# Optimization experiments

Hardware: AMD Instinct MI355X
Metric: run time of the kernel (lower is better)

Reference implementation:

```python
import jax, jax.numpy as jnp
import numpy as np

B, Hm, Wm, Dm = 1, 32, 32, 32
N = Hm * Wm * Dm
C = 128
HEADS, DH = 8, 16
G = 32
L = 2
OUT = 1


def _ln(x, g, b):
    mu = jnp.mean(x, -1, keepdims=True)
    var = jnp.mean((x - mu) ** 2, -1, keepdims=True)
    return (x - mu) * jax.lax.rsqrt(var + 1e-5) * g + b


def setup_inputs() -> dict:
    key = jax.random.key(0)
    ks = iter(jax.random.split(key, 64))
    def nrm(shape, s=0.02):
        return jax.random.normal(next(ks), shape, jnp.float32) * s
    return {
        "x": jax.random.normal(next(ks), (B, N, 3), jnp.float32),
        "fx": jax.random.normal(next(ks), (B, N, 1), jnp.float32),
        "pre_w1": nrm((4, 2 * C)), "pre_b1": jnp.zeros((2 * C,), jnp.float32),
        "pre_w2": nrm((2 * C, C)), "pre_b2": jnp.zeros((C,), jnp.float32),
        "placeholder": jax.random.uniform(next(ks), (C,), jnp.float32) / C,
        "ln1_g": jnp.ones((L, C), jnp.float32), "ln1_b": jnp.zeros((L, C), jnp.float32),
        "convx_w": nrm((L, C, C, 3, 3, 3)), "convx_b": jnp.zeros((L, C), jnp.float32),
        "convfx_w": nrm((L, C, C, 3, 3, 3)), "convfx_b": jnp.zeros((L, C), jnp.float32),
        "slice_w": nrm((L, DH, G), 0.1), "slice_b": jnp.zeros((L, G), jnp.float32),
        "temperature": jnp.full((L, 1, HEADS, 1, 1), 0.5, jnp.float32),
        "wq": nrm((L, DH, DH), 0.1), "wk": nrm((L, DH, DH), 0.1), "wv": nrm((L, DH, DH), 0.1),
        "wo": nrm((L, HEADS * DH, C)), "bo": jnp.zeros((L, C), jnp.float32),
        "ln2_g": jnp.ones((L, C), jnp.float32), "ln2_b": jnp.zeros((L, C), jnp.float32),
        "mlp_w1": nrm((L, C, C)), "mlp_b1": jnp.zeros((L, C), jnp.float32),
        "mlp_w2": nrm((L, C, C)), "mlp_b2": jnp.zeros((L, C), jnp.float32),
        "ln3_g": jnp.ones((C,), jnp.float32), "ln3_b": jnp.zeros((C,), jnp.float32),
        "out_w": nrm((C, OUT)), "out_b": jnp.zeros((OUT,), jnp.float32),
    }


def _conv3d(x, w, b):
    # x: [B,C,H,W,D], w: [O,I,3,3,3], SAME padding (kernel//2) as torch Conv3d
    y = jax.lax.conv_general_dilated(x, w, (1, 1, 1), "SAME",
                                     dimension_numbers=("NCDHW", "OIDHW", "NCDHW"))
    return y + b[None, :, None, None, None]


def _physics_attn(z, cw_x, cb_x, cw_fx, cb_fx, sw, sb, temp, wq, wk, wv, wo, bo):
    # z: [B, N, C] -> structured mesh conv projections -> slice attention
    xg = z.reshape(B, Hm, Wm, Dm, C).transpose(0, 4, 1, 2, 3)  # [B,C,H,W,D]

    def split_heads(t):  # [B,I,H,W,D] -> [B,heads,N,dh]
        return t.transpose(0, 2, 3, 4, 1).reshape(B, N, HEADS, DH).transpose(0, 2, 1, 3)

    x_mid = split_heads(_conv3d(xg, cw_x, cb_x))
    fx_mid = split_heads(_conv3d(xg, cw_fx, cb_fx))
    # slice assignment weights: [B,heads,N,G], temperature-scaled softmax
    slice_logits = (x_mid @ sw + sb) / temp
    swt = jax.nn.softmax(slice_logits, axis=-1)
    norm = jnp.sum(swt, axis=2)  # [B,heads,G]
    tok = jnp.einsum("bhnc,bhng->bhgc", fx_mid, swt) / (norm + 1e-5)[..., None]
    q, k, v = tok @ wq, tok @ wk, tok @ wv  # [B,heads,G,dh]
    attn = jax.nn.softmax((q @ k.transpose(0, 1, 3, 2)) * (DH ** -0.5), axis=-1)
    ot = attn @ v  # [B,heads,G,dh]
    out = jnp.einsum("bhgc,bhng->bhnc", ot, swt)  # de-slice back to tokens
    out = out.transpose(0, 2, 1, 3).reshape(B, N, HEADS * DH)
    return out @ wo + bo


def reference(x, fx, pre_w1, pre_b1, pre_w2, pre_b2, placeholder,
              ln1_g, ln1_b, convx_w, convx_b, convfx_w, convfx_b,
              slice_w, slice_b, temperature, wq, wk, wv, wo, bo,
              ln2_g, ln2_b, mlp_w1, mlp_b1, mlp_w2, mlp_b2,
              ln3_g, ln3_b, out_w, out_b):
    h = jnp.concatenate([x, fx], axis=-1)  # [B,N,space+fun]
    z = jax.nn.gelu(h @ pre_w1 + pre_b1, approximate=False) @ pre_w2 + pre_b2 + placeholder
    for l in range(L):
        zn = _ln(z, ln1_g[l], ln1_b[l])
        z = _physics_attn(zn, convx_w[l], convx_b[l], convfx_w[l], convfx_b[l],
                          slice_w[l], slice_b[l], temperature[l],
                          wq[l], wk[l], wv[l], wo[l], bo[l]) + z
        zn = _ln(z, ln2_g[l], ln2_b[l])
        z = jax.nn.gelu(zn @ mlp_w1[l] + mlp_b1[l], approximate=False) @ mlp_w2[l] + mlp_b2[l] + z
    return _ln(z, ln3_g, ln3_b) @ out_w + out_b
```

## Files before the change

kernel.cpp:

```cpp
#include <hip/hip_runtime.h>
#include <hip/hip_bf16.h>

#define DEV __device__ __forceinline__

constexpr int N   = 32768;
constexpr int TOTAL_IN = 2038481;

constexpr int OFF_X        = 0;
constexpr int OFF_FX       = 98304;
constexpr int OFF_PRE_W1   = 131072;
constexpr int OFF_PRE_B1   = 132096;
constexpr int OFF_PRE_W2   = 132352;
constexpr int OFF_PRE_B2   = 165120;
constexpr int OFF_PLACE    = 165248;
constexpr int OFF_LN1_G    = 165376;
constexpr int OFF_LN1_B    = 165632;
constexpr int OFF_CONVX_W  = 165888;
constexpr int OFF_CONVX_B  = 1050624;
constexpr int OFF_CONVFX_W = 1050880;
constexpr int OFF_CONVFX_B = 1935616;
constexpr int OFF_SLICE_W  = 1935872;
constexpr int OFF_SLICE_B  = 1936896;
constexpr int OFF_TEMP     = 1936960;
constexpr int OFF_WQ       = 1936976;
constexpr int OFF_WK       = 1937488;
constexpr int OFF_WV       = 1938000;
constexpr int OFF_WO       = 1938512;
constexpr int OFF_BO       = 1971280;
constexpr int OFF_LN2_G    = 1971536;
constexpr int OFF_LN2_B    = 1971792;
constexpr int OFF_MLP_W1   = 1972048;
constexpr int OFF_MLP_B1   = 2004816;
constexpr int OFF_MLP_W2   = 2005072;
constexpr int OFF_MLP_B2   = 2037840;
constexpr int OFF_LN3_G    = 2038096;
constexpr int OFF_LN3_B    = 2038224;
constexpr int OFF_OUT_W    = 2038352;
constexpr int OFF_OUT_B    = 2038480;

__device__ __constant__ int d_PRE[32] = {
  0, 98304, 131072, 132096, 132352, 165120, 165248, 165376, 165632,
  165888, 1050624, 1050880, 1935616, 1935872, 1936896, 1936960, 1936976,
  1937488, 1938000, 1938512, 1971280, 1971536, 1971792, 1972048, 2004816,
  2005072, 2037840, 2038096, 2038224, 2038352, 2038480, 2038481
};

constexpr size_t F_IN   = 16;
constexpr size_t F_WT   = 2038512;
constexpr size_t F_Z    = F_WT   + 1769472;
constexpr size_t F_ZN   = F_Z    + 4194304;
constexpr size_t F_CONV = F_ZN   + 4194304;
constexpr size_t F_SWT  = F_CONV + 8388608;
constexpr size_t F_TOKP = F_SWT  + 8388608;
constexpr size_t F_TOK2 = F_TOKP + 1114112;
constexpr size_t F_WP   = F_TOK2 + 34816;
constexpr size_t F_END  = F_WP   + 65536;

struct InPtrs { const void* p[31]; };

typedef short short8v  __attribute__((ext_vector_type(8)));
typedef float float4v  __attribute__((ext_vector_type(4)));
#define MFMA16(A,B,C) __builtin_amdgcn_mfma_f32_16x16x32_bf16(A,B,C,0,0,0)

DEV float geluf(float x) { return 0.5f * x * (1.0f + erff(x * 0.70710678118654752f)); }
DEV short f2bs(float x) { union { __hip_bfloat16 h; short s; } c; c.h = __float2bfloat16(x); return c.s; }

__global__ void k_setup(InPtrs ptrs, float* __restrict__ ws,
                        short* __restrict__ wtf, short* __restrict__ wp) {
  const bool isbf = (*(const unsigned*)ptrs.p[15] == 0x3F003F00u);
  int b = blockIdx.x, tid = threadIdx.x;
  if (b < 512) {
    int stride = 512 * 256;
    for (int e = b * 256 + tid; e < TOTAL_IN; e += stride) {
      if ((e >= OFF_CONVX_W && e < OFF_CONVX_B) || (e >= OFF_CONVFX_W && e < OFF_CONVFX_B)) continue;
      int lo = 0, hi = 30;
#pragma unroll
      for (int it = 0; it < 5; ++it) {
        int mid = (lo + hi + 1) >> 1;
        if (e >= d_PRE[mid]) lo = mid; else hi = mid - 1;
      }
      int loc = e - d_PRE[lo];
      float v;
      if (isbf) {
        unsigned short u = ((const unsigned short*)ptrs.p[lo])[loc];
        v = __uint_as_float(((unsigned)u) << 16);
      } else {
        v = ((const float*)ptrs.p[lo])[loc];
      }
      ws[F_IN + e] = v;
    }
  } else if (b < 1376) {
    int f = (b - 512) * 256 + tid;
    int lane = f & 63;
    int rest = f >> 6;
    int ntile = rest & 15;
    int r2 = rest >> 4;
    int layer = r2 / 108;
    int kt = r2 - layer * 108;
    int icb = kt / 27, tap = kt - icb * 27;
    int oc = ntile * 16 + (lane & 15);
    int ic0 = icb * 32 + (lane >> 4) * 8;
    const void* cw = (oc < 128) ? ptrs.p[9] : ptrs.p[11];
    int o = oc & 127;
    size_t base = ((size_t)(layer * 128 + o) * 128) * 27 + tap;
    short8v out;
    if (isbf) {
      const unsigned short* src = (const unsigned short*)cw + base;
#pragma unroll
      for (int j = 0; j < 8; ++j) out[j] = (short)src[(size_t)(ic0 + j) * 27];
    } else {
      const float* src = (const float*)cw + base;
#pragma unroll
      for (int j = 0; j < 8; ++j) out[j] = f2bs(src[(size_t)(ic0 + j) * 27]);
    }
    *(short8v*)(wtf + (size_t)f * 8) = out;
  } else {
    int f = (b - 1376) * 256 + tid;
    int lane = f & 63;
    int t = f >> 6;
    const void* srcb; size_t soff; int kt, nt;
    if (t < 64) { srcb = ptrs.p[4]; soff = 0; kt = t >> 3; nt = t & 7; }
    else {
      int r = t - 64, l = r / 96, r2 = r - l * 96;
      int which = r2 >> 5, idx2 = r2 & 31;
      kt = idx2 >> 3; nt = idx2 & 7;
      srcb = (which == 0 ? ptrs.p[23] : (which == 1 ? ptrs.p[25] : ptrs.p[19]));
      soff = (size_t)l * 16384;
    }
    int k0 = kt * 32 + (lane >> 4) * 8;
    int n = nt * 16 + (lane & 15);
    size_t base = soff + (size_t)k0 * 128 + n;
    short8v out;
    if (isbf) {
      const unsigned short* src = (const unsigned short*)srcb + base;
#pragma unroll
      for (int j = 0; j < 8; ++j) out[j] = (short)src[(size_t)j * 128];
    } else {
      const float* src = (const float*)srcb + base;
#pragma unroll
      for (int j = 0; j < 8; ++j) out[j] = f2bs(src[(size_t)j * 128]);
    }
    *(short8v*)(wp + (size_t)f * 8) = out;
  }
}

__global__ __launch_bounds__(256)
void k_prenet(const float* __restrict__ ip, const short* __restrict__ wp,
              float* __restrict__ z, short* __restrict__ znb) {
  __shared__ float w1s[1024], b1s[256], cvec[128], g1s[128], be1s[128];
  __shared__ float xv[64][4];
  __shared__ __align__(16) short ts[64 * 264];
  int tid = threadIdx.x;
  int wv = tid >> 6, lane = tid & 63;
  int m = lane & 15, q = lane >> 4;
  int n0 = blockIdx.x * 64;
  for (int i = tid; i < 1024; i += 256) w1s[i] = ip[OFF_PRE_W1 + i];
  b1s[tid] = ip[OFF_PRE_B1 + tid];
  if (tid < 128) {
    cvec[tid] = ip[OFF_PRE_B2 + tid] + ip[OFF_PLACE + tid];
    g1s[tid]  = ip[OFF_LN1_G + tid];
    be1s[tid] = ip[OFF_LN1_B + tid];
  }
  if (tid < 64) {
    xv[tid][0] = ip[OFF_X + (n0 + tid) * 3 + 0];
    xv[tid][1] = ip[OFF_X + (n0 + tid) * 3 + 1];
    xv[tid][2] = ip[OFF_X + (n0 + tid) * 3 + 2];
    xv[tid][3] = ip[OFF_FX + n0 + tid];
  }
  __syncthreads();
  {
    float w0 = w1s[tid], wA = w1s[256 + tid], wB = w1s[512 + tid], wC = w1s[768 + tid];
    float bb = b1s[tid];
    for (int t = 0; t < 64; ++t) {
      float hv = bb + xv[t][0] * w0 + xv[t][1] * wA + xv[t][2] * wB + xv[t][3] * wC;
      ts[t * 264 + tid] = f2bs(geluf(hv));
    }
  }
  __syncthreads();
  const short8v* pwf = (const short8v*)wp;
  float4v acc[8];
#pragma unroll
  for (int nt = 0; nt < 8; ++nt) acc[nt] = (float4v){0.f, 0.f, 0.f, 0.f};
  for (int kt = 0; kt < 8; ++kt) {
    short8v A = *(const short8v*)(ts + (wv * 16 + m) * 264 + kt * 32 + q * 8);
#pragma unroll
    for (int nt = 0; nt < 8; ++nt)
      acc[nt] = MFMA16(A, pwf[(kt * 8 + nt) * 64 + lane], acc[nt]);
  }
  float vz[8][4];
#pragma unroll
  for (int nt = 0; nt < 8; ++nt) {
    int col = nt * 16 + m;
#pragma unroll
    for (int r = 0; r < 4; ++r) {
      vz[nt][r] = acc[nt][r] + cvec[col];
      z[(size_t)(n0 + wv * 16 + q * 4 + r) * 128 + col] = vz[nt][r];
    }
  }
#pragma unroll
  for (int r = 0; r < 4; ++r) {
    float s1 = 0.f, s2 = 0.f;
#pragma unroll
    for (int nt = 0; nt < 8; ++nt) { float v = vz[nt][r]; s1 += v; s2 += v * v; }
#pragma unroll
    for (int off = 1; off < 16; off <<= 1) { s1 += __shfl_xor(s1, off); s2 += __shfl_xor(s2, off); }
    float mu = s1 * (1.0f / 128.0f);
    float var = s2 * (1.0f / 128.0f) - mu * mu;
    float rst = 1.0f / sqrtf(var + 1e-5f);
    size_t rowb = (size_t)(n0 + wv * 16 + q * 4 + r) * 128;
#pragma unroll
    for (int nt = 0; nt < 8; ++nt) {
      int col = nt * 16 + m;
      znb[rowb + col] = f2bs((vz[nt][r] - mu) * rst * g1s[col] + be1s[col]);
    }
  }
}

__global__ __launch_bounds__(256)
void k_conv(const float* __restrict__ ip, const short* __restrict__ znb,
            const short* __restrict__ wtf, float* __restrict__ cv, int layer) {
  __shared__ __align__(16) short halo[15360];
  int tid = threadIdx.x;
  int wv = tid >> 6, lane = tid & 63;
  int m = lane & 15, q = lane >> 4;
  int n0 = blockIdx.x * 64;
  int h = n0 >> 10, w0 = (n0 >> 5) & 31;
  float bias_r[4];
#pragma unroll
  for (int nt = 0; nt < 4; ++nt) {
    int oc = (wv * 4 + nt) * 16 + m;
    bias_r[nt] = (oc < 128) ? ip[OFF_CONVX_B + layer * 128 + oc]
                            : ip[OFF_CONVFX_B + layer * 128 + (oc - 128)];
  }
  float4v acc[4][4];
#pragma unroll
  for (int a = 0; a < 4; ++a)
#pragma unroll
    for (int b = 0; b < 4; ++b) acc[a][b] = (float4v){0.f, 0.f, 0.f, 0.f};

  const short8v* wf = (const short8v*)wtf + (size_t)layer * 110592 + (wv * 4) * 64 + lane;
  short8v bc0 = wf[0], bc1 = wf[64], bc2 = wf[128], bc3 = wf[192];

  int tap = 0, icb = 0;
  for (int kt = 0; kt < 108; ++kt) {
    if (tap == 0) {
      __syncthreads();
      for (int i = tid; i < 1632; i += 256) {
        int pr = i >> 2, qq = i & 3;
        int line = pr / 34, dpos = pr - line * 34;
        int hh2 = h + (line >> 2) - 1, ww2 = w0 + (line & 3) - 1, dd2 = dpos - 1;
        short8v v = (short8v){0, 0, 0, 0, 0, 0, 0, 0};
        if (((unsigned)hh2 < 32u) && ((unsigned)ww2 < 32u) && ((unsigned)dd2 < 32u)) {
          int tok = (hh2 << 10) + (ww2 << 5) + dd2;
          v = *(const short8v*)(znb + (size_t)tok * 128 + icb * 32 + qq * 8);
        }
        *(short8v*)(halo + qq * 3840 + (line * 40 + dpos) * 8) = v;
      }
      __syncthreads();
    }
    int ktn = (kt + 1 < 108) ? kt + 1 : kt;
    const short8v* wn = wf + (size_t)ktn * 1024;
    short8v bn0 = wn[0], bn1 = wn[64], bn2 = wn[128], bn3 = wn[192];

    int ta = tap / 9, rem = tap - ta * 9, tb = rem / 3, tc = rem - tb * 3;
    const short* hp = halo + q * 3840 + ((ta * 4 + tb) * 40 + tc + m) * 8;
    short8v A0 = *(const short8v*)(hp);
    short8v A1 = *(const short8v*)(hp + 128);
    short8v A2 = *(const short8v*)(hp + 320);
    short8v A3 = *(const short8v*)(hp + 448);

    acc[0][0] = MFMA16(A0, bc0, acc[0][0]);
    acc[1][0] = MFMA16(A1, bc0, acc[1][0]);
    acc[2][0] = MFMA16(A2, bc0, acc[2][0]);
    acc[3][0] = MFMA16(A3, bc0, acc[3][0]);
    acc[0][1] = MFMA16(A0, bc1, acc[0][1]);
    acc[1][1] = MFMA16(A1, bc1, acc[1][1]);
    acc[2][1] = MFMA16(A2, bc1, acc[2][1]);
    acc[3][1] = MFMA16(A3, bc1, acc[3][1]);
    acc[0][2] = MFMA16(A0, bc2, acc[0][2]);
    acc[1][2] = MFMA16(A1, bc2, acc[1][2]);
    acc[2][2] = MFMA16(A2, bc2, acc[2][2]);
    acc[3][2] = MFMA16(A3, bc2, acc[3][2]);
    acc[0][3] = MFMA16(A0, bc3, acc[0][3]);
    acc[1][3] = MFMA16(A1, bc3, acc[1][3]);
    acc[2][3] = MFMA16(A2, bc3, acc[2][3]);
    acc[3][3] = MFMA16(A3, bc3, acc[3][3]);

    bc0 = bn0; bc1 = bn1; bc2 = bn2; bc3 = bn3;
    if (++tap == 27) { tap = 0; ++icb; }
  }
#pragma unroll
  for (int mt = 0; mt < 4; ++mt) {
    float* cp = cv + (size_t)(n0 + mt * 16 + q * 4) * 256 + (wv * 4) * 16 + m;
#pragma unroll
    for (int nt = 0; nt < 4; ++nt) {
#pragma unroll
      for (int r = 0; r < 4; ++r)
        cp[(size_t)r * 256 + nt * 16] = acc[mt][nt][r] + bias_r[nt];
    }
  }
}

__global__ __launch_bounds__(256)
void k_slice(const float* __restrict__ ip, const float* __restrict__ cv,
             short* __restrict__ swtb, float* __restrict__ tokp, int layer) {
  __shared__ float sws[512], sbs[32], its[8];
  __shared__ float swl[32 * 257];
  __shared__ float fxl[32 * 128];
  int tid = threadIdx.x;
  for (int i = tid; i < 512; i += 256) sws[i] = ip[OFF_SLICE_W + layer * 512 + i];
  if (tid < 32) sbs[tid] = ip[OFF_SLICE_B + layer * 32 + tid];
  if (tid < 8)  its[tid] = 1.0f / ip[OFF_TEMP + layer * 8 + tid];
  float4 ta0 = make_float4(0,0,0,0), ta1 = ta0, ta2 = ta0, ta3 = ta0;
  float np = 0.f;
  for (int s = 0; s < 4; ++s) {
    int tbase = blockIdx.x * 128 + s * 32;
    __syncthreads();
    for (int i = tid; i < 1024; i += 256) {
      int t = i >> 5, c4 = (i & 31) * 4;
      *(float4*)&fxl[t * 128 + c4] = *(const float4*)&cv[(size_t)(tbase + t) * 256 + 128 + c4];
    }
    {
      int t = tid >> 3, hh = tid & 7;
      float xm[16];
#pragma unroll
      for (int qq = 0; qq < 4; ++qq)
        *(float4*)&xm[qq * 4] = *(const float4*)&cv[(size_t)(tbase + t) * 256 + hh * 16 + qq * 4];
      float lg[32];
      float itv = its[hh];
#pragma unroll
      for (int g = 0; g < 32; ++g) {
        float sacc = sbs[g];
#pragma unroll
        for (int j = 0; j < 16; ++j) sacc += xm[j] * sws[j * 32 + g];
        lg[g] = sacc * itv;
      }
      float mx = -1e30f;
#pragma unroll
      for (int g = 0; g < 32; ++g) mx = fmaxf(mx, lg[g]);
      float sum = 0.f;
#pragma unroll
      for (int g = 0; g < 32; ++g) { lg[g] = expf(lg[g] - mx); sum += lg[g]; }
      float inv = 1.0f / sum;
#pragma unroll
      for (int g = 0; g < 32; ++g) {
        lg[g] *= inv;
        swl[t * 257 + hh * 32 + g] = lg[g];
      }
#pragma unroll
      for (int qq = 0; qq < 4; ++qq) {
        short8v pk;
#pragma unroll
        for (int j = 0; j < 8; ++j) pk[j] = f2bs(lg[qq * 8 + j]);
        *(short8v*)(swtb + (size_t)(tbase + t) * 256 + hh * 32 + qq * 8) = pk;
      }
    }
    __syncthreads();
    {
      int ah = tid >> 5, ag = tid & 31;
      for (int t2 = 0; t2 < 32; ++t2) {
        float sv = swl[t2 * 257 + ah * 32 + ag];
        np += sv;
        const float* f = &fxl[t2 * 128 + ah * 16];
        float4 f0 = *(const float4*)&f[0], f1 = *(const float4*)&f[4];
        float4 f2 = *(const float4*)&f[8], f3 = *(const float4*)&f[12];
        ta0.x += sv * f0.x; ta0.y += sv * f0.y; ta0.z += sv * f0.z; ta0.w += sv * f0.w;
        ta1.x += sv * f1.x; ta1.y += sv * f1.y; ta1.z += sv * f1.z; ta1.w += sv * f1.w;
        ta2.x += sv * f2.x; ta2.y += sv * f2.y; ta2.z += sv * f2.z; ta2.w += sv * f2.w;
        ta3.x += sv * f3.x; ta3.y += sv * f3.y; ta3.z += sv * f3.z; ta3.w += sv * f3.w;
      }
    }
  }
  int ah = tid >> 5, ag = tid & 31;
  size_t base = (size_t)blockIdx.x * 4352 + (size_t)(ah * 32 + ag) * 16;
  *(float4*)&tokp[base + 0]  = ta0;
  *(float4*)&tokp[base + 4]  = ta1;
  *(float4*)&tokp[base + 8]  = ta2;
  *(float4*)&tokp[base + 12] = ta3;
  tokp[(size_t)blockIdx.x * 4352 + 4096 + ah * 32 + ag] = np;
}

__global__ void k_tokred1(const float* __restrict__ tokp, float* __restrict__ tok2) {
  int ogrp = blockIdx.x % 17, bgrp = blockIdx.x / 17;
  int o = ogrp * 256 + threadIdx.x;
  float s = 0.f;
  int b0 = bgrp * 32;
#pragma unroll 8
  for (int b = b0; b < b0 + 32; ++b) s += tokp[(size_t)b * 4352 + o];
  tok2[(size_t)bgrp * 4352 + o] = s;
}

__global__ __launch_bounds__(256)
void k_fused(const float* __restrict__ ip, const short* __restrict__ swtb,
             const float* __restrict__ tok2, const short* __restrict__ wp,
             float* __restrict__ z, short* __restrict__ znb,
             void* __restrict__ dout, const void* __restrict__ tempraw, int layer) {
  __shared__ __align__(16) char smem[64512];
  short* otb = (short*)smem;
  float* bia = (float*)(smem + 8192);
  float* trs = (float*)(smem + 12288);
  short* znt = (short*)(smem + 12288);
  float* kk  = (float*)(smem + 29696);
  short* al  = (short*)(smem + 29696);
  float* vvs = (float*)(smem + 47104);
  float* bol = bia, *b1s = bia + 128, *b2s = bia + 256, *g2s = bia + 384;
  float* be2s = bia + 512, *lng = bia + 640, *lnb = bia + 768, *ows = bia + 896;
  int tid = threadIdx.x;
  int wv = tid >> 6, lane = tid & 63;
  int m = lane & 15, q = lane >> 4;
  int n0 = blockIdx.x * 64;
  if (tid < 128) {
    bol[tid]  = ip[OFF_BO + layer * 128 + tid];
    b1s[tid]  = ip[OFF_MLP_B1 + layer * 128 + tid];
    b2s[tid]  = ip[OFF_MLP_B2 + layer * 128 + tid];
    g2s[tid]  = ip[OFF_LN2_G + layer * 128 + tid];
    be2s[tid] = ip[OFF_LN2_B + layer * 128 + tid];
    if (layer == 0) {
      lng[tid] = ip[OFF_LN1_G + 128 + tid];
      lnb[tid] = ip[OFF_LN1_B + 128 + tid];
      ows[tid] = 0.f;
    } else {
      lng[tid] = ip[OFF_LN3_G + tid];
      lnb[tid] = ip[OFF_LN3_B + tid];
      ows[tid] = ip[OFF_OUT_W + tid];
    }
  }
  for (int i = tid; i < 4352; i += 256) {
    float s = 0.f;
#pragma unroll
    for (int b = 0; b < 8; ++b) s += tok2[(size_t)b * 4352 + i];
    trs[i] = s;
  }
  __syncthreads();
  float qv[16];
  {
    const float* wqp = ip + OFF_WQ + layer * 256;
    const float* wkp = ip + OFF_WK + layer * 256;
    const float* wvp = ip + OFF_WV + layer * 256;
    float inv = 1.0f / (trs[4096 + tid] + 1e-5f);
    float t[16];
#pragma unroll
    for (int c = 0; c < 16; ++c) t[c] = trs[tid * 16 + c] * inv;
#pragma unroll
    for (int c = 0; c < 16; ++c) {
      float aq = 0.f, ak = 0.f, av = 0.f;
#pragma unroll
      for (int j = 0; j < 16; ++j) {
        float tv = t[j];
        aq += tv * wqp[j * 16 + c];
        ak += tv * wkp[j * 16 + c];
        av += tv * wvp[j * 16 + c];
      }
      qv[c] = aq;
      kk[tid * 17 + c] = ak;
      vvs[tid * 17 + c] = av;
    }
  }
  __syncthreads();
  {
    int hh = tid >> 5, g = tid & 31;
    float sc[32];
    float mx = -1e30f;
#pragma unroll
    for (int g2 = 0; g2 < 32; ++g2) {
      float s = 0.f;
#pragma unroll
      for (int c = 0; c < 16; ++c) s += qv[c] * kk[(hh * 32 + g2) * 17 + c];
      s *= 0.25f;
      sc[g2] = s; mx = fmaxf(mx, s);
    }
    float sum = 0.f;
#pragma unroll
    for (int g2 = 0; g2 < 32; ++g2) { sc[g2] = expf(sc[g2] - mx); sum += sc[g2]; }
    float inv2 = 1.0f / sum;
    float o[16];
#pragma unroll
    for (int c = 0; c < 16; ++c) o[c] = 0.f;
#pragma unroll
    for (int g2 = 0; g2 < 32; ++g2) {
      float p = sc[g2] * inv2;
#pragma unroll
      for (int c = 0; c < 16; ++c) o[c] += p * vvs[(hh * 32 + g2) * 17 + c];
    }
#pragma unroll
    for (int dh = 0; dh < 16; ++dh)
      otb[hh * 512 + (((g >> 3) * 16 + dh) << 3) + (g & 7)] = f2bs(o[dh]);
  }
  __syncthreads();
  float4v accd[8];
#pragma unroll
  for (int h = 0; h < 8; ++h) accd[h] = (float4v){0.f, 0.f, 0.f, 0.f};
#pragma unroll
  for (int h = 0; h < 8; ++h) {
    short8v A = *(const short8v*)(swtb + (size_t)(n0 + wv * 16 + m) * 256 + h * 32 + q * 8);
    accd[h] = MFMA16(A, *(const short8v*)(otb + h * 512 + lane * 8), accd[h]);
  }
  __syncthreads();
#pragma unroll
  for (int h = 0; h < 8; ++h)
#pragma unroll
    for (int r = 0; r < 4; ++r)
      al[(wv * 16 + q * 4 + r) * 136 + h * 16 + m] = f2bs(accd[h][r]);
  __syncthreads();
  const short8v* wof = (const short8v*)(wp + (size_t)(128 + 96 * layer) * 512);
  float4v a2[8];
#pragma unroll
  for (int nt = 0; nt < 8; ++nt) a2[nt] = (float4v){0.f, 0.f, 0.f, 0.f};
  for (int kt = 0; kt < 4; ++kt) {
    short8v A = *(const short8v*)(al + (wv * 16 + m) * 136 + kt * 32 + q * 8);
#pragma unroll
    for (int nt = 0; nt < 8; ++nt)
      a2[nt] = MFMA16(A, wof[(kt * 8 + nt) * 64 + lane], a2[nt]);
  }
  float vmid[8][4];
#pragma unroll
  for (int nt = 0; nt < 8; ++nt) {
    int col = nt * 16 + m;
#pragma unroll
    for (int r = 0; r < 4; ++r)
      vmid[nt][r] = z[(size_t)(n0 + wv * 16 + q * 4 + r) * 128 + col] + a2[nt][r] + bol[col];
  }
#pragma unroll
  for (int r = 0; r < 4; ++r) {
    float s1 = 0.f, s2 = 0.f;
#pragma unroll
    for (int nt = 0; nt < 8; ++nt) { float v = vmid[nt][r]; s1 += v; s2 += v * v; }
#pragma unroll
    for (int off = 1; off < 16; off <<= 1) { s1 += __shfl_xor(s1, off); s2 += __shfl_xor(s2, off); }
    float mu = s1 * (1.0f / 128.0f);
    float var = s2 * (1.0f / 128.0f) - mu * mu;
    float rst = 1.0f / sqrtf(var + 1e-5f);
#pragma unroll
    for (int nt = 0; nt < 8; ++nt) {
      int col = nt * 16 + m;
      znt[(wv * 16 + q * 4 + r) * 136 + col] = f2bs((vmid[nt][r] - mu) * rst * g2s[col] + be2s[col]);
    }
  }
  __syncthreads();
  const short8v* w1f = (const short8v*)(wp + (size_t)(64 + 96 * layer) * 512);
  const short8v* w2f = (const short8v*)(wp + (size_t)(96 + 96 * layer) * 512);
  float4v acc[8];
#pragma unroll
  for (int nt = 0; nt < 8; ++nt) acc[nt] = (float4v){0.f, 0.f, 0.f, 0.f};
  for (int kt = 0; kt < 4; ++kt) {
    short8v A = *(const short8v*)(znt + (wv * 16 + m) * 136 + kt * 32 + q * 8);
#pragma unroll
    for (int nt = 0; nt < 8; ++nt)
      acc[nt] = MFMA16(A, w1f[(kt * 8 + nt) * 64 + lane], acc[nt]);
  }
  __syncthreads();
#pragma unroll
  for (int nt = 0; nt < 8; ++nt) {
    int col = nt * 16 + m;
#pragma unroll
    for (int r = 0; r < 4; ++r)
      al[(wv * 16 + q * 4 + r) * 136 + col] = f2bs(geluf(acc[nt][r] + b1s[col]));
  }
  __syncthreads();
  float4v a4[8];
#pragma unroll
  for (int nt = 0; nt < 8; ++nt) a4[nt] = (float4v){0.f, 0.f, 0.f, 0.f};
  for (int kt = 0; kt < 4; ++kt) {
    short8v A = *(const short8v*)(al + (wv * 16 + m) * 136 + kt * 32 + q * 8);
#pragma unroll
    for (int nt = 0; nt < 8; ++nt)
      a4[nt] = MFMA16(A, w2f[(kt * 8 + nt) * 64 + lane], a4[nt]);
  }
  float vfin[8][4];
#pragma unroll
  for (int nt = 0; nt < 8; ++nt) {
    int col = nt * 16 + m;
#pragma unroll
    for (int r = 0; r < 4; ++r) {
      vfin[nt][r] = vmid[nt][r] + a4[nt][r] + b2s[col];
      z[(size_t)(n0 + wv * 16 + q * 4 + r) * 128 + col] = vfin[nt][r];
    }
  }
#pragma unroll
  for (int r = 0; r < 4; ++r) {
    float s1 = 0.f, s2 = 0.f;
#pragma unroll
    for (int nt = 0; nt < 8; ++nt) { float v = vfin[nt][r]; s1 += v; s2 += v * v; }
#pragma unroll
    for (int off = 1; off < 16; off <<= 1) { s1 += __shfl_xor(s1, off); s2 += __shfl_xor(s2, off); }
    float mu = s1 * (1.0f / 128.0f);
    float var = s2 * (1.0f / 128.0f) - mu * mu;
    float rst = 1.0f / sqrtf(var + 1e-5f);
    int n = n0 + wv * 16 + q * 4 + r;
    if (layer == 0) {
      size_t rowb = (size_t)n * 128;
#pragma unroll
      for (int nt = 0; nt < 8; ++nt) {
        int col = nt * 16 + m;
        znb[rowb + col] = f2bs((vfin[nt][r] - mu) * rst * lng[col] + lnb[col]);
      }
    } else {
      float contrib = 0.f;
#pragma unroll
      for (int nt = 0; nt < 8; ++nt) {
        int col = nt * 16 + m;
        contrib += ((vfin[nt][r] - mu) * rst * lng[col] + lnb[col]) * ows[col];
      }
#pragma unroll
      for (int off = 1; off < 16; off <<= 1) contrib += __shfl_xor(contrib, off);
      if (m == 0) {
        float res = contrib + ip[OFF_OUT_B];
        unsigned tw = *(const unsigned*)tempraw;
        if (tw == 0x3F003F00u) ((__hip_bfloat16*)dout)[n] = __float2bfloat16(res);
        else                   ((float*)dout)[n] = res;
      }
    }
  }
}

extern "C" void kernel_launch(void* const* d_in, const int* in_sizes, int n_in,
                              void* d_out, int out_size, void* d_ws, size_t ws_size,
                              hipStream_t stream) {
  (void)in_sizes; (void)out_size; (void)ws_size;
  if (n_in < 31) return;
  float* ws   = (float*)d_ws;
  float* ip   = ws + F_IN;
  short* wtf  = (short*)(ws + F_WT);
  float* z    = ws + F_Z;
  short* znb  = (short*)(ws + F_ZN);
  float* cv   = ws + F_CONV;
  short* swtb = (short*)(ws + F_SWT);
  float* tkp  = ws + F_TOKP;
  float* tk2  = ws + F_TOK2;
  short* wp   = (short*)(ws + F_WP);

  InPtrs P;
  for (int i = 0; i < 31; ++i) P.p[i] = d_in[i];

  k_setup <<<1440, 256, 0, stream>>>(P, ws, wtf, wp);
  k_prenet<<<512, 256, 0, stream>>>(ip, wp, z, znb);
  for (int l = 0; l < 2; ++l) {
    k_conv   <<<512, 256, 0, stream>>>(ip, znb, wtf, cv, l);
    k_slice  <<<256, 256, 0, stream>>>(ip, cv, swtb, tkp, l);
    k_tokred1<<<136, 256, 0, stream>>>(tkp, tk2);
    k_fused  <<<512, 256, 0, stream>>>(ip, swtb, tk2, wp, z, znb, d_out, d_in[15], l);
  }
}
```

Baseline: 441.8 us.

## Fuse slice softmax and token aggregation into conv epilogue; stage weight repack via LDS

```diff
diff --git a/kernel.cpp b/kernel.cpp
--- a/kernel.cpp
+++ b/kernel.cpp
@@ -49,11 +49,10 @@
 constexpr size_t F_WT   = 2038512;
 constexpr size_t F_Z    = F_WT   + 1769472;
 constexpr size_t F_ZN   = F_Z    + 4194304;
-constexpr size_t F_CONV = F_ZN   + 4194304;
-constexpr size_t F_SWT  = F_CONV + 8388608;
-constexpr size_t F_TOKP = F_SWT  + 8388608;
-constexpr size_t F_TOK2 = F_TOKP + 1114112;
-constexpr size_t F_WP   = F_TOK2 + 34816;
+constexpr size_t F_TOKP = F_ZN   + 4194304;
+constexpr size_t F_SWT  = F_TOKP + 8388608;
+constexpr size_t F_TOK2 = F_SWT  + 8388608;
+constexpr size_t F_WP   = F_TOK2 + 69632;
 constexpr size_t F_END  = F_WP   + 65536;
 
 struct InPtrs { const void* p[31]; };
@@ -64,9 +63,11 @@
 
 DEV float geluf(float x) { return 0.5f * x * (1.0f + erff(x * 0.70710678118654752f)); }
 DEV short f2bs(float x) { union { __hip_bfloat16 h; short s; } c; c.h = __float2bfloat16(x); return c.s; }
+DEV float bs2f(short s) { union { unsigned u; float f; } c; c.u = ((unsigned)(unsigned short)s) << 16; return c.f; }
 
 __global__ void k_setup(InPtrs ptrs, float* __restrict__ ws,
                         short* __restrict__ wtf, short* __restrict__ wp) {
+  __shared__ short wl[13952];
   const bool isbf = (*(const unsigned*)ptrs.p[15] == 0x3F003F00u);
   int b = blockIdx.x, tid = threadIdx.x;
   if (b < 512) {
@@ -89,33 +90,33 @@
       }
       ws[F_IN + e] = v;
     }
-  } else if (b < 1376) {
-    int f = (b - 512) * 256 + tid;
-    int lane = f & 63;
-    int rest = f >> 6;
-    int ntile = rest & 15;
-    int r2 = rest >> 4;
-    int layer = r2 / 108;
-    int kt = r2 - layer * 108;
-    int icb = kt / 27, tap = kt - icb * 27;
-    int oc = ntile * 16 + (lane & 15);
-    int ic0 = icb * 32 + (lane >> 4) * 8;
-    const void* cw = (oc < 128) ? ptrs.p[9] : ptrs.p[11];
-    int o = oc & 127;
-    size_t base = ((size_t)(layer * 128 + o) * 128) * 27 + tap;
-    short8v out;
-    if (isbf) {
-      const unsigned short* src = (const unsigned short*)cw + base;
-#pragma unroll
-      for (int j = 0; j < 8; ++j) out[j] = (short)src[(size_t)(ic0 + j) * 27];
-    } else {
-      const float* src = (const float*)cw + base;
-#pragma unroll
-      for (int j = 0; j < 8; ++j) out[j] = f2bs(src[(size_t)(ic0 + j) * 27]);
-    }
-    *(short8v*)(wtf + (size_t)f * 8) = out;
+  } else if (b < 640) {
+    int idx = b - 512;
+    int layer = idx >> 6, rem = idx & 63;
+    int icb = rem >> 4, ntile = rem & 15;
+    for (int i = tid; i < 13824; i += 256) {
+      int oc_r = i / 864, off = i - oc_r * 864;
+      int oc = ntile * 16 + oc_r;
+      const void* cw = (oc < 128) ? ptrs.p[9] : ptrs.p[11];
+      size_t base = ((size_t)(layer * 128 + (oc & 127)) * 128 + icb * 32) * 27 + off;
+      wl[oc_r * 872 + off] = isbf ? (short)((const unsigned short*)cw)[base]
+                                  : f2bs(((const float*)cw)[base]);
+    }
+    __syncthreads();
+    int wv = tid >> 6, lane = tid & 63;
+    int m = lane & 15, q = lane >> 4;
+    for (int tg = 0; tg < 7; ++tg) {
+      int tap = tg * 4 + wv;
+      if (tap < 27) {
+        short8v out;
+#pragma unroll
+        for (int j = 0; j < 8; ++j) out[j] = wl[m * 872 + (q * 8 + j) * 27 + tap];
+        size_t f = ((size_t)((layer * 108 + icb * 27 + tap) * 16 + ntile)) * 64 + lane;
+        *(short8v*)(wtf + f * 8) = out;
+      }
+    }
   } else {
-    int f = (b - 1376) * 256 + tid;
+    int f = (b - 640) * 256 + tid;
     int lane = f & 63;
     int t = f >> 6;
     const void* srcb; size_t soff; int kt, nt;
@@ -218,8 +219,16 @@
 
 __global__ __launch_bounds__(256)
 void k_conv(const float* __restrict__ ip, const short* __restrict__ znb,
-            const short* __restrict__ wtf, float* __restrict__ cv, int layer) {
-  __shared__ __align__(16) short halo[15360];
+            const short* __restrict__ wtf, short* __restrict__ swtb,
+            float* __restrict__ tokp, int layer) {
+  __shared__ __align__(16) char cs[35840];
+  short* halo = (short*)cs;
+  float* sws = (float*)cs;
+  float* sbs = (float*)(cs + 2048);
+  float* its = (float*)(cs + 2176);
+  short* xl  = (short*)(cs + 2224);
+  short* fxl = (short*)(cs + 10672);
+  short* swl = (short*)(cs + 19120);
   int tid = threadIdx.x;
   int wv = tid >> 6, lane = tid & 63;
   int m = lane & 15, q = lane >> 4;
@@ -289,43 +298,35 @@
     bc0 = bn0; bc1 = bn1; bc2 = bn2; bc3 = bn3;
     if (++tap == 27) { tap = 0; ++icb; }
   }
-#pragma unroll
-  for (int mt = 0; mt < 4; ++mt) {
-    float* cp = cv + (size_t)(n0 + mt * 16 + q * 4) * 256 + (wv * 4) * 16 + m;
-#pragma unroll
-    for (int nt = 0; nt < 4; ++nt) {
-#pragma unroll
-      for (int r = 0; r < 4; ++r)
-        cp[(size_t)r * 256 + nt * 16] = acc[mt][nt][r] + bias_r[nt];
-    }
-  }
-}
-
-__global__ __launch_bounds__(256)
-void k_slice(const float* __restrict__ ip, const float* __restrict__ cv,
-             short* __restrict__ swtb, float* __restrict__ tokp, int layer) {
-  __shared__ float sws[512], sbs[32], its[8];
-  __shared__ float swl[32 * 257];
-  __shared__ float fxl[32 * 128];
-  int tid = threadIdx.x;
+  __syncthreads();
   for (int i = tid; i < 512; i += 256) sws[i] = ip[OFF_SLICE_W + layer * 512 + i];
   if (tid < 32) sbs[tid] = ip[OFF_SLICE_B + layer * 32 + tid];
   if (tid < 8)  its[tid] = 1.0f / ip[OFF_TEMP + layer * 8 + tid];
   float4 ta0 = make_float4(0,0,0,0), ta1 = ta0, ta2 = ta0, ta3 = ta0;
   float np = 0.f;
-  for (int s = 0; s < 4; ++s) {
-    int tbase = blockIdx.x * 128 + s * 32;
+  for (int half = 0; half < 2; ++half) {
+#pragma unroll
+    for (int mh = 0; mh < 2; ++mh) {
+      int mt = half * 2 + mh;
+      int rowb = mh * 16 + q * 4;
+#pragma unroll
+      for (int nt = 0; nt < 4; ++nt) {
+        int ct = wv * 4 + nt;
+        short* dst = (ct < 8) ? xl : fxl;
+        int col = (ct & 7) * 16 + m;
+#pragma unroll
+        for (int r = 0; r < 4; ++r)
+          dst[(rowb + r) * 132 + col] = f2bs(acc[mt][nt][r] + bias_r[nt]);
+      }
+    }
     __syncthreads();
-    for (int i = tid; i < 1024; i += 256) {
-      int t = i >> 5, c4 = (i & 31) * 4;
-      *(float4*)&fxl[t * 128 + c4] = *(const float4*)&cv[(size_t)(tbase + t) * 256 + 128 + c4];
-    }
     {
-      int t = tid >> 3, hh = tid & 7;
+      int tl = tid >> 3, hh = tid & 7;
       float xm[16];
-#pragma unroll
-      for (int qq = 0; qq < 4; ++qq)
-        *(float4*)&xm[qq * 4] = *(const float4*)&cv[(size_t)(tbase + t) * 256 + hh * 16 + qq * 4];
+      short8v x0 = *(const short8v*)(xl + tl * 132 + hh * 16);
+      short8v x1 = *(const short8v*)(xl + tl * 132 + hh * 16 + 8);
+#pragma unroll
+      for (int j = 0; j < 8; ++j) { xm[j] = bs2f(x0[j]); xm[8 + j] = bs2f(x1[j]); }
       float lg[32];
       float itv = its[hh];
 #pragma unroll
@@ -342,42 +343,40 @@
 #pragma unroll
       for (int g = 0; g < 32; ++g) { lg[g] = expf(lg[g] - mx); sum += lg[g]; }
       float inv = 1.0f / sum;
+      short pk16[32];
 #pragma unroll
       for (int g = 0; g < 32; ++g) {
-        lg[g] *= inv;
-        swl[t * 257 + hh * 32 + g] = lg[g];
-      }
-#pragma unroll
-      for (int qq = 0; qq < 4; ++qq) {
-        short8v pk;
-#pragma unroll
-        for (int j = 0; j < 8; ++j) pk[j] = f2bs(lg[qq * 8 + j]);
-        *(short8v*)(swtb + (size_t)(tbase + t) * 256 + hh * 32 + qq * 8) = pk;
-      }
+        short sv = f2bs(lg[g] * inv);
+        pk16[g] = sv;
+        swl[tl * 257 + hh * 32 + g] = sv;
+      }
+      int token = n0 + half * 32 + tl;
+#pragma unroll
+      for (int qq = 0; qq < 4; ++qq)
+        *(short8v*)(swtb + (size_t)token * 256 + hh * 32 + qq * 8) = *(short8v*)&pk16[qq * 8];
     }
     __syncthreads();
     {
-      int ah = tid >> 5, ag = tid & 31;
+      int hh2 = tid >> 5, g2 = tid & 31;
       for (int t2 = 0; t2 < 32; ++t2) {
-        float sv = swl[t2 * 257 + ah * 32 + ag];
+        float sv = bs2f(swl[t2 * 257 + hh2 * 32 + g2]);
         np += sv;
-        const float* f = &fxl[t2 * 128 + ah * 16];
-        float4 f0 = *(const float4*)&f[0], f1 = *(const float4*)&f[4];
-        float4 f2 = *(const float4*)&f[8], f3 = *(const float4*)&f[12];
-        ta0.x += sv * f0.x; ta0.y += sv * f0.y; ta0.z += sv * f0.z; ta0.w += sv * f0.w;
-        ta1.x += sv * f1.x; ta1.y += sv * f1.y; ta1.z += sv * f1.z; ta1.w += sv * f1.w;
-        ta2.x += sv * f2.x; ta2.y += sv * f2.y; ta2.z += sv * f2.z; ta2.w += sv * f2.w;
-        ta3.x += sv * f3.x; ta3.y += sv * f3.y; ta3.z += sv * f3.z; ta3.w += sv * f3.w;
-      }
-    }
-  }
-  int ah = tid >> 5, ag = tid & 31;
-  size_t base = (size_t)blockIdx.x * 4352 + (size_t)(ah * 32 + ag) * 16;
+        short8v f0 = *(const short8v*)(fxl + t2 * 132 + hh2 * 16);
+        short8v f1 = *(const short8v*)(fxl + t2 * 132 + hh2 * 16 + 8);
+        ta0.x += sv * bs2f(f0[0]); ta0.y += sv * bs2f(f0[1]); ta0.z += sv * bs2f(f0[2]); ta0.w += sv * bs2f(f0[3]);
+        ta1.x += sv * bs2f(f0[4]); ta1.y += sv * bs2f(f0[5]); ta1.z += sv * bs2f(f0[6]); ta1.w += sv * bs2f(f0[7]);
+        ta2.x += sv * bs2f(f1[0]); ta2.y += sv * bs2f(f1[1]); ta2.z += sv * bs2f(f1[2]); ta2.w += sv * bs2f(f1[3]);
+        ta3.x += sv * bs2f(f1[4]); ta3.y += sv * bs2f(f1[5]); ta3.z += sv * bs2f(f1[6]); ta3.w += sv * bs2f(f1[7]);
+      }
+    }
+    __syncthreads();
+  }
+  size_t base = (size_t)blockIdx.x * 4352 + (size_t)tid * 16;
   *(float4*)&tokp[base + 0]  = ta0;
   *(float4*)&tokp[base + 4]  = ta1;
   *(float4*)&tokp[base + 8]  = ta2;
   *(float4*)&tokp[base + 12] = ta3;
-  tokp[(size_t)blockIdx.x * 4352 + 4096 + ah * 32 + ag] = np;
+  tokp[(size_t)blockIdx.x * 4352 + 4096 + tid] = np;
 }
 
 __global__ void k_tokred1(const float* __restrict__ tokp, float* __restrict__ tok2) {
@@ -428,7 +427,7 @@
   for (int i = tid; i < 4352; i += 256) {
     float s = 0.f;
 #pragma unroll
-    for (int b = 0; b < 8; ++b) s += tok2[(size_t)b * 4352 + i];
+    for (int b = 0; b < 16; ++b) s += tok2[(size_t)b * 4352 + i];
     trs[i] = s;
   }
   __syncthreads();
@@ -623,21 +622,19 @@
   short* wtf  = (short*)(ws + F_WT);
   float* z    = ws + F_Z;
   short* znb  = (short*)(ws + F_ZN);
-  float* cv   = ws + F_CONV;
+  float* tkp  = ws + F_TOKP;
   short* swtb = (short*)(ws + F_SWT);
-  float* tkp  = ws + F_TOKP;
   float* tk2  = ws + F_TOK2;
   short* wp   = (short*)(ws + F_WP);
 
   InPtrs P;
   for (int i = 0; i < 31; ++i) P.p[i] = d_in[i];
 
-  k_setup <<<1440, 256, 0, stream>>>(P, ws, wtf, wp);
+  k_setup <<<704, 256, 0, stream>>>(P, ws, wtf, wp);
   k_prenet<<<512, 256, 0, stream>>>(ip, wp, z, znb);
   for (int l = 0; l < 2; ++l) {
-    k_conv   <<<512, 256, 0, stream>>>(ip, znb, wtf, cv, l);
-    k_slice  <<<256, 256, 0, stream>>>(ip, cv, swtb, tkp, l);
-    k_tokred1<<<136, 256, 0, stream>>>(tkp, tk2);
+    k_conv   <<<512, 256, 0, stream>>>(ip, znb, wtf, swtb, tkp, l);
+    k_tokred1<<<272, 256, 0, stream>>>(tkp, tk2);
     k_fused  <<<512, 256, 0, stream>>>(ip, swtb, tk2, wp, z, znb, d_out, d_in[15], l);
   }
 }
```

Result: slower. 1.240 ms (+180.6%).
